# Kernel optimization log

Measured on AMD Instinct MI355X. Metric: run time of the kernel, lower is better.

The kernel has to match this reference:

```python
import jax, jax.numpy as jnp
import numpy as np

B, S, E = 4, 2048, 1024

def setup_inputs() -> dict:
    key = jax.random.key(0)
    ks = jax.random.split(key, 6)
    values = jax.random.normal(ks[0], (B, S, E), dtype=jnp.float32)
    keys_t = jax.random.normal(ks[1], (B, S, E), dtype=jnp.float32)
    query = jax.random.normal(ks[2], (B, S, E), dtype=jnp.float32)
    mask = jax.random.randint(ks[3], (B, 1, S), 0, 2, dtype=jnp.int32)
    W_out = jax.random.normal(ks[4], (E, E), dtype=jnp.float32) * (1.0 / np.sqrt(E))
    b_out = jax.random.normal(ks[5], (E,), dtype=jnp.float32) * 0.01
    return {"values": values, "keys": keys_t, "query": query, "mask": mask,
            "W_out": W_out, "b_out": b_out}

def reference(values, keys, query, mask, W_out, b_out):
    # scores: [B, S, S] = Q K^T / sqrt(embed_size)  (NOTE: module scales by
    # sqrt(embed_size), not sqrt(head_dim), and never applies q/k/v Linears)
    scale = 1.0 / jnp.sqrt(jnp.asarray(E, dtype=query.dtype))
    scores = jnp.einsum('bqe,bke->bqk', query, keys) * scale
    scores = jnp.where(mask == 0, -jnp.inf, scores)  # masked_fill(mask==0, -inf)
    attn = jax.nn.softmax(scores, axis=-1)
    out = jnp.einsum('bqk,bke->bqe', attn, values)
    # fc_out: torch Linear -> x @ W^T + b
    return out @ W_out.T + b_out
```

## Files before the change

### kernel.cpp

```cpp
#include <hip/hip_runtime.h>

#define BB 4
#define SS 2048
#define EE 1024

typedef _Float16 f16;
typedef _Float16 f16x4 __attribute__((ext_vector_type(4)));
typedef _Float16 f16x8 __attribute__((ext_vector_type(8)));
typedef float f32x4 __attribute__((ext_vector_type(4)));

typedef const __attribute__((address_space(1))) void* gas_ptr;
typedef __attribute__((address_space(3))) void* las_ptr;

__device__ __forceinline__ void gl_lds16(const void* g, void* l) {
  __builtin_amdgcn_global_load_lds((gas_ptr)g, (las_ptr)l, 16, 0, 0);
}

#define BAR() __builtin_amdgcn_s_barrier()
#define PRIO1() __builtin_amdgcn_s_setprio(1)
#define PRIO0() __builtin_amdgcn_s_setprio(0)
#define WAITV6() asm volatile("s_waitcnt vmcnt(6)" ::: "memory")
#define WAITV0() asm volatile("s_waitcnt vmcnt(0)" ::: "memory")

__global__ __launch_bounds__(256) void prep(const int* __restrict__ mask,
                                            int* __restrict__ pos,
                                            int2* __restrict__ cnt,
                                            f16* __restrict__ Kc,
                                            f16* __restrict__ Vc) {
  const int b = blockIdx.x, t = threadIdx.x;
  const int* mb = mask + b * SS;
  int4 a0 = ((const int4*)mb)[t * 2];
  int4 a1 = ((const int4*)mb)[t * 2 + 1];
  int m[8] = {a0.x, a0.y, a0.z, a0.w, a1.x, a1.y, a1.z, a1.w};
  int tot = 0;
#pragma unroll
  for (int j = 0; j < 8; ++j) tot += m[j];
  __shared__ int sc[256];
  sc[t] = tot;
  __syncthreads();
  for (int off = 1; off < 256; off <<= 1) {
    int v = (t >= off) ? sc[t - off] : 0;
    __syncthreads();
    sc[t] += v;
    __syncthreads();
  }
  const int count = sc[255];
  const int padded = (count + 127) & ~127;
  int run = sc[t] - tot;
#pragma unroll
  for (int j = 0; j < 8; ++j) {
    pos[b * SS + t * 8 + j] = run;
    run += m[j];
  }
  if (t == 0) cnt[b] = make_int2(count, padded);
  const int nz = (padded - count) * 128;
  f16x8 z = {};
  for (int i = t; i < nz; i += 256) {
    int r = count + (i >> 7), cc = i & 127;
    ((f16x8*)(Kc + ((long)b * SS + r) * EE))[cc] = z;
    ((f16x8*)(Vc + ((long)b * SS + r) * EE))[cc] = z;
  }
}

__global__ __launch_bounds__(256) void prep2(const float* __restrict__ Q,
                                             const float* __restrict__ W,
                                             const float* __restrict__ K,
                                             const float* __restrict__ V,
                                             const int* __restrict__ mask,
                                             const int* __restrict__ pos,
                                             const int2* __restrict__ cnt,
                                             f16* __restrict__ Qh,
                                             f16* __restrict__ Wh,
                                             f16* __restrict__ Kc,
                                             f16* __restrict__ Vc,
                                             float* __restrict__ rowsum,
                                             int* __restrict__ items,
                                             int* __restrict__ nit) {
  const int x = blockIdx.x, t = threadIdx.x;
  if (x < 4608) {
    const float* in = (x < 4096) ? Q : W;
    f16* out = (x < 4096) ? Qh : Wh;
    long i = (long)(x < 4096 ? x : x - 4096) * 256 + t;
    float4 v0 = ((const float4*)in)[i * 2];
    float4 v1 = ((const float4*)in)[i * 2 + 1];
    f16x8 o;
    o[0] = (f16)v0.x; o[1] = (f16)v0.y; o[2] = (f16)v0.z; o[3] = (f16)v0.w;
    o[4] = (f16)v1.x; o[5] = (f16)v1.y; o[6] = (f16)v1.z; o[7] = (f16)v1.w;
    ((f16x8*)out)[i] = o;
    return;
  }
  if (x == 4608) {
    float4 z = {0.f, 0.f, 0.f, 0.f};
#pragma unroll
    for (int r = 0; r < 8; ++r) ((float4*)rowsum)[t + r * 256] = z;
    return;
  }
  if (x == 4609) {
    if (t < 8) {
      int nbx[4];
#pragma unroll
      for (int zz = 0; zz < 4; ++zz) nbx[zz] = cnt[zz].y >> 7;
      int mxn = nbx[0];
#pragma unroll
      for (int zz = 1; zz < 4; ++zz) mxn = nbx[zz] > mxn ? nbx[zz] : mxn;
      const int mx = 6 * mxn;
      const int bz = t >> 1, half = t & 1;
      int g = 0;
      for (int q = 0; q < 4; ++q)
        for (int bx = 0; bx < nbx[bz]; ++bx)
          items[(g++ << 3) | t] = bx | ((half * 4 + q) << 8) | (bz << 16);
      for (int q = 0; q < 2; ++q)
        for (int bx = 0; bx < nbx[bz]; ++bx)
          items[(g++ << 3) | t] = bx | ((half * 2 + q) << 8) | (bz << 16) | (1 << 24);
      for (; g < mx; ++g) items[(g << 3) | t] = (3 << 24);
      if (t == 0) nit[0] = mx << 3;
    }
    return;
  }
  const int r = x - 4610, b = r >> 11, s = r & (SS - 1);
  if (!mask[b * SS + s]) return;
  const int p = pos[b * SS + s];
  float4 kv = ((const float4*)(K + ((long)b * SS + s) * EE))[t];
  float4 vv = ((const float4*)(V + ((long)b * SS + s) * EE))[t];
  f16x4 ko, vo;
  ko[0] = (f16)kv.x; ko[1] = (f16)kv.y; ko[2] = (f16)kv.z; ko[3] = (f16)kv.w;
  vo[0] = (f16)vv.x; vo[1] = (f16)vv.y; vo[2] = (f16)vv.z; vo[3] = (f16)vv.w;
  ((f16x4*)(Kc + ((long)b * SS + p) * EE))[t] = ko;
  ((f16x4*)(Vc + ((long)b * SS + p) * EE))[t] = vo;
}

__device__ __forceinline__ void stage64(const f16* g, long K, f16* l, int h, int t) {
  int rr = t >> 3, sp = t & 7;
  int row = h * 64 + rr;
  int sl = sp ^ (rr & 7);
  gl_lds16(g + (long)row * K + (sl << 3), (char*)l + ((row << 6) + (sp << 3)) * 2);
}

__device__ __forceinline__ void read_a(f16x8 (&d)[4][2], const f16* base, int q,
                                       int wm, int l15, int l4) {
#pragma unroll
  for (int mf = 0; mf < 4; ++mf)
#pragma unroll
    for (int kk = 0; kk < 2; ++kk) {
      int row = wm * 128 + (q * 4 + mf) * 16 + l15;
      int sl = kk * 4 + l4;
      d[mf][kk] = *(const f16x8*)(base + row * 64 + ((sl ^ (row & 7)) << 3));
    }
}

__device__ __forceinline__ void read_b1(f16x8 (&d)[2], const f16* base, int f,
                                        int wn, int l15, int l4) {
#pragma unroll
  for (int kk = 0; kk < 2; ++kk) {
    int row = wn * 32 + f * 16 + l15;
    int sl = kk * 4 + l4;
    d[kk] = *(const f16x8*)(base + row * 64 + ((sl ^ (row & 7)) << 3));
  }
}

__device__ __forceinline__ void mfma_n(f32x4 (&acc)[8][2], const f16x8 (&Af)[4][2],
                                       const f16x8 (&Bf)[2], int q, int f) {
#pragma unroll
  for (int mf = 0; mf < 4; ++mf)
#pragma unroll
    for (int kk = 0; kk < 2; ++kk)
      acc[q * 4 + mf][f] = __builtin_amdgcn_mfma_f32_16x16x32_f16(
          Af[mf][kk], Bf[kk], acc[q * 4 + mf][f], 0, 0, 0);
}

__device__ __forceinline__ void n128_core(f32x4 (&acc)[8][2], const f16* Ag,
                                          const f16* Bg, long L, int NT,
                                          f16* lds, int tid, int wm, int wn,
                                          int l15, int l4) {
  f16* As0 = lds;
  f16* As1 = lds + 16384;
  f16* Bs0 = lds + 32768;
  f16* Bs1 = lds + 40960;
  f16x8 a[4][2], b[2], b2[2];
  const int NIT = NT >> 1;

  stage64(Bg, L, Bs0, 0, tid); stage64(Bg, L, Bs0, 1, tid);
#pragma unroll
  for (int h = 0; h < 4; ++h) stage64(Ag, L, As0, h, tid);
  stage64(Bg + 64, L, Bs1, 0, tid); stage64(Bg + 64, L, Bs1, 1, tid);
#pragma unroll
  for (int h = 0; h < 4; ++h) stage64(Ag + 64, L, As1, h, tid);
  WAITV6();
  BAR();

  for (int i = 0; i < NIT; ++i) {
    int t2 = 2 * i + 2, t3 = 2 * i + 3;
    long k2 = (long)((t2 < NT) ? t2 : NT - 1) << 6;
    long k3 = (long)((t3 < NT) ? t3 : NT - 1) << 6;
    read_a(a, As0, 0, wm, l15, l4);
    read_b1(b, Bs0, 0, wn, l15, l4);
    BAR(); PRIO1(); mfma_n(acc, a, b, 0, 0); PRIO0(); BAR();
    read_b1(b2, Bs0, 1, wn, l15, l4);
    BAR(); PRIO1(); mfma_n(acc, a, b2, 0, 1); PRIO0(); BAR();
    read_a(a, As0, 1, wm, l15, l4);
    stage64(Bg + k2, L, Bs0, 0, tid); stage64(Bg + k2, L, Bs0, 1, tid);
    BAR(); PRIO1(); mfma_n(acc, a, b2, 1, 1); PRIO0(); BAR();
#pragma unroll
    for (int h = 0; h < 4; ++h) stage64(Ag + k2, L, As0, h, tid);
    BAR(); PRIO1(); mfma_n(acc, a, b, 1, 0); PRIO0();
    WAITV6();
    BAR();
    read_a(a, As1, 0, wm, l15, l4);
    read_b1(b, Bs1, 0, wn, l15, l4);
    BAR(); PRIO1(); mfma_n(acc, a, b, 0, 0); PRIO0(); BAR();
    read_b1(b2, Bs1, 1, wn, l15, l4);
    BAR(); PRIO1(); mfma_n(acc, a, b2, 0, 1); PRIO0(); BAR();
    read_a(a, As1, 1, wm, l15, l4);
    stage64(Bg + k3, L, Bs1, 0, tid); stage64(Bg + k3, L, Bs1, 1, tid);
    BAR(); PRIO1(); mfma_n(acc, a, b2, 1, 1); PRIO0(); BAR();
#pragma unroll
    for (int h = 0; h < 4; ++h) stage64(Ag + k3, L, As1, h, tid);
    BAR(); PRIO1(); mfma_n(acc, a, b, 1, 0); PRIO0();
    WAITV6();
    BAR();
  }
  WAITV0();
}

__global__ __launch_bounds__(512, 1) void uber(const f16* __restrict__ Qh,
                                               const f16* __restrict__ Kc,
                                               const f16* __restrict__ Vc,
                                               const f16* __restrict__ Wh,
                                               f16* __restrict__ P,
                                               f16* __restrict__ VWt,
                                               float* __restrict__ rowsum,
                                               const int2* __restrict__ cnt,
                                               const int* __restrict__ items,
                                               const int* __restrict__ nit) {
  extern __shared__ f16 lds[];
  const int tid = threadIdx.x;
  const int lane = tid & 63, wv = tid >> 6;
  const int wm = wv >> 2, wn = wv & 3;
  const int l15 = lane & 15, l4 = lane >> 4;
  const int n = nit[0];

  for (int idx = blockIdx.x; idx < n; idx += 256) {
    const int it = items[idx];
    const int kind = (it >> 24) & 3;
    if (kind == 3) continue;
    const int bx = it & 255, by = (it >> 8) & 255, bz = (it >> 16) & 255;
    const long m0 = (long)by * 256;
    const long n0 = (long)bx * 128;
    const f16* Ag = kind ? (Wh + m0 * EE) : (Qh + (long)bz * SS * EE + m0 * EE);
    const f16* Bg = (kind ? Vc : Kc) + (long)bz * SS * EE + n0 * EE;

    f32x4 acc[8][2] = {};
    n128_core(acc, Ag, Bg, EE, EE >> 6, lds, tid, wm, wn, l15, l4);

    const long crow = m0 + wm * 128 + l4 * 4;
    const long ccol = n0 + wn * 32 + l15;
    if (kind == 0) {
      const int count = cnt[bz].x;
      f16* Co = P + (long)bz * SS * SS;
      float* rs = rowsum + (bz << 11);
      const float scale = 1.0f / 32.0f;
      int mv[2];
#pragma unroll
      for (int nf = 0; nf < 2; ++nf) mv[nf] = (ccol + nf * 16) < count;
#pragma unroll
      for (int mf = 0; mf < 8; ++mf)
#pragma unroll
        for (int jj = 0; jj < 4; ++jj) {
          float rp = 0.f;
#pragma unroll
          for (int nf = 0; nf < 2; ++nf) {
            float p = mv[nf] ? __expf(acc[mf][nf][jj] * scale) : 0.f;
            Co[(crow + mf * 16 + jj) * SS + ccol + nf * 16] = (f16)p;
            rp += p;
          }
          rp += __shfl_xor(rp, 1); rp += __shfl_xor(rp, 2);
          rp += __shfl_xor(rp, 4); rp += __shfl_xor(rp, 8);
          if (l15 == 0) atomicAdd(&rs[crow + mf * 16 + jj], rp);
        }
    } else {
      f16* Co = VWt + (long)bz * EE * SS;
#pragma unroll
      for (int mf = 0; mf < 8; ++mf)
#pragma unroll
        for (int nf = 0; nf < 2; ++nf)
#pragma unroll
          for (int jj = 0; jj < 4; ++jj)
            Co[(crow + mf * 16 + jj) * SS + ccol + nf * 16] = (f16)acc[mf][nf][jj];
    }
  }
}

__global__ __launch_bounds__(512, 1) void pv128(const f16* __restrict__ P,
                                                const f16* __restrict__ VWt,
                                                float* __restrict__ out,
                                                const float* __restrict__ bias,
                                                const float* __restrict__ rowsum,
                                                const int2* __restrict__ cnt) {
  extern __shared__ f16 lds[];
  const int d = blockIdx.x;
  const int x = d & 7, r = d >> 3;
  const int bz = x >> 1;
  const int by = (x & 1) * 4 + (r & 3);
  const int bx = r >> 2;
  int2 cc = cnt[bz];
  const int padded = cc.y;
  if (padded <= 0) return;
  const long m0 = (long)by * 256;
  const long n0 = (long)bx * 128;
  const int tid = threadIdx.x;
  const int lane = tid & 63, wv = tid >> 6;
  const int wm = wv >> 2, wn = wv & 3;
  const int l15 = lane & 15, l4 = lane >> 4;
  const f16* Ag = P + (long)bz * SS * SS + m0 * SS;
  const f16* Bg = VWt + (long)bz * EE * SS + n0 * SS;

  f32x4 acc[8][2] = {};
  n128_core(acc, Ag, Bg, SS, padded >> 6, lds, tid, wm, wn, l15, l4);

  const long crow = m0 + wm * 128 + l4 * 4;
  const long ccol = n0 + wn * 32 + l15;
  float* Co = out + (long)bz * SS * EE;
  const float* rs = rowsum + (bz << 11);
  float bv[2];
#pragma unroll
  for (int nf = 0; nf < 2; ++nf) bv[nf] = bias[ccol + nf * 16];
#pragma unroll
  for (int mf = 0; mf < 8; ++mf)
#pragma unroll
    for (int jj = 0; jj < 4; ++jj) {
      float inv = 1.f / rs[crow + mf * 16 + jj];
#pragma unroll
      for (int nf = 0; nf < 2; ++nf)
        Co[(crow + mf * 16 + jj) * EE + ccol + nf * 16] =
            acc[mf][nf][jj] * inv + bv[nf];
    }
}

extern "C" void kernel_launch(void* const* d_in, const int* in_sizes, int n_in,
                              void* d_out, int out_size, void* d_ws, size_t ws_size,
                              hipStream_t stream) {
  const float* V = (const float*)d_in[0];
  const float* Kin = (const float*)d_in[1];
  const float* Q = (const float*)d_in[2];
  const int* mask = (const int*)d_in[3];
  const float* W = (const float*)d_in[4];
  const float* bias = (const float*)d_in[5];
  float* out = (float*)d_out;

  const long NE = (long)BB * SS * EE;
  f16* Qh = (f16*)d_ws;
  f16* Kc = Qh + NE;
  f16* Vc = Kc + NE;
  f16* Wh = Vc + NE;
  f16* VWt = Wh + (long)EE * EE;
  f16* P = VWt + NE;
  float* rowsum = (float*)(P + (long)BB * SS * SS);
  int* pos = (int*)(rowsum + (long)BB * SS);
  int2* cnt = (int2*)(pos + (long)BB * SS);
  int* items = (int*)(cnt + BB);
  int* nit = items + 1024;

  const size_t LDS_N = 98304;
  hipFuncSetAttribute((const void*)uber, hipFuncAttributeMaxDynamicSharedMemorySize, LDS_N);
  hipFuncSetAttribute((const void*)pv128, hipFuncAttributeMaxDynamicSharedMemorySize, LDS_N);

  prep<<<BB, 256, 0, stream>>>(mask, pos, cnt, Kc, Vc);
  prep2<<<4610 + BB * SS, 256, 0, stream>>>(Q, W, Kin, V, mask, pos, cnt,
                                            Qh, Wh, Kc, Vc, rowsum, items, nit);
  uber<<<256, 512, LDS_N, stream>>>(Qh, Kc, Vc, Wh, P, VWt, rowsum, cnt, items, nit);
  pv128<<<256, 512, LDS_N, stream>>>(P, VWt, out, bias, rowsum, cnt);
}
```

Measured before the change: 102.6 us.

## Widen uber GEMM tiles to 256x256 with new pipelined core

Replaces the 256x128 GEMM core in the persistent uber kernel with a 256x256 core (g256_core). Each wave now computes a 128x64 sub-tile, and A and B are double-buffered in 128KB of LDS. Key/value padding and work-item counts move to 256-column granularity. The aim is to raise arithmetic intensity and cut redundant A-tile loads. In exchange it uses more accumulator registers and more LDS, adds padding work when the mask count is not a multiple of 256, and leaves fewer items to balance across the 256 blocks.

```diff
diff --git a/kernel.cpp b/kernel.cpp
--- a/kernel.cpp
+++ b/kernel.cpp
@@ -19,7 +19,9 @@
 #define BAR() __builtin_amdgcn_s_barrier()
 #define PRIO1() __builtin_amdgcn_s_setprio(1)
 #define PRIO0() __builtin_amdgcn_s_setprio(0)
+#define WAITV8() asm volatile("s_waitcnt vmcnt(8)" ::: "memory")
 #define WAITV6() asm volatile("s_waitcnt vmcnt(6)" ::: "memory")
+#define WAITV4() asm volatile("s_waitcnt vmcnt(4)" ::: "memory")
 #define WAITV0() asm volatile("s_waitcnt vmcnt(0)" ::: "memory")
 
 __global__ __launch_bounds__(256) void prep(const int* __restrict__ mask,
@@ -45,7 +47,7 @@
     __syncthreads();
   }
   const int count = sc[255];
-  const int padded = (count + 127) & ~127;
+  const int padded = (count + 255) & ~255;
   int run = sc[t] - tot;
 #pragma unroll
   for (int j = 0; j < 8; ++j) {
@@ -99,7 +101,7 @@
     if (t < 8) {
       int nbx[4];
 #pragma unroll
-      for (int zz = 0; zz < 4; ++zz) nbx[zz] = cnt[zz].y >> 7;
+      for (int zz = 0; zz < 4; ++zz) nbx[zz] = cnt[zz].y >> 8;
       int mxn = nbx[0];
 #pragma unroll
       for (int zz = 1; zz < 4; ++zz) mxn = nbx[zz] > mxn ? nbx[zz] : mxn;
@@ -148,6 +150,18 @@
     }
 }
 
+__device__ __forceinline__ void read_b2(f16x8 (&d)[2][2], const f16* base, int nh,
+                                        int wn, int l15, int l4) {
+#pragma unroll
+  for (int nf = 0; nf < 2; ++nf)
+#pragma unroll
+    for (int kk = 0; kk < 2; ++kk) {
+      int row = wn * 64 + (nh * 2 + nf) * 16 + l15;
+      int sl = kk * 4 + l4;
+      d[nf][kk] = *(const f16x8*)(base + row * 64 + ((sl ^ (row & 7)) << 3));
+    }
+}
+
 __device__ __forceinline__ void read_b1(f16x8 (&d)[2], const f16* base, int f,
                                         int wn, int l15, int l4) {
 #pragma unroll
@@ -158,6 +172,18 @@
   }
 }
 
+__device__ __forceinline__ void mfma_q(f32x4 (&acc)[8][4], const f16x8 (&Af)[4][2],
+                                       const f16x8 (&Bf)[2][2], int q, int nh) {
+#pragma unroll
+  for (int mf = 0; mf < 4; ++mf)
+#pragma unroll
+    for (int nf = 0; nf < 2; ++nf)
+#pragma unroll
+      for (int kk = 0; kk < 2; ++kk)
+        acc[q * 4 + mf][nh * 2 + nf] = __builtin_amdgcn_mfma_f32_16x16x32_f16(
+            Af[mf][kk], Bf[nf][kk], acc[q * 4 + mf][nh * 2 + nf], 0, 0, 0);
+}
+
 __device__ __forceinline__ void mfma_n(f32x4 (&acc)[8][2], const f16x8 (&Af)[4][2],
                                        const f16x8 (&Bf)[2], int q, int f) {
 #pragma unroll
@@ -166,6 +192,64 @@
     for (int kk = 0; kk < 2; ++kk)
       acc[q * 4 + mf][f] = __builtin_amdgcn_mfma_f32_16x16x32_f16(
           Af[mf][kk], Bf[kk], acc[q * 4 + mf][f], 0, 0, 0);
+}
+
+__device__ __forceinline__ void g256_core(f32x4 (&acc)[8][4], const f16* Ag,
+                                          const f16* Bg, long L, int NT,
+                                          f16* lds, int tid, int wm, int wn,
+                                          int l15, int l4) {
+  f16* As0 = lds;
+  f16* As1 = lds + 16384;
+  f16* Bs0 = lds + 32768;
+  f16* Bs1 = lds + 49152;
+  f16x8 a[4][2], b[2][2], b2[2][2];
+  const int NIT = NT >> 1;
+
+#pragma unroll
+  for (int h = 0; h < 4; ++h) stage64(Bg, L, Bs0, h, tid);
+#pragma unroll
+  for (int h = 0; h < 4; ++h) stage64(Ag, L, As0, h, tid);
+#pragma unroll
+  for (int h = 0; h < 4; ++h) stage64(Bg + 64, L, Bs1, h, tid);
+#pragma unroll
+  for (int h = 0; h < 4; ++h) stage64(Ag + 64, L, As1, h, tid);
+  WAITV8();
+  BAR();
+
+  for (int i = 0; i < NIT; ++i) {
+    int t2 = 2 * i + 2, t3 = 2 * i + 3;
+    long k2 = (long)((t2 < NT) ? t2 : NT - 1) << 6;
+    long k3 = (long)((t3 < NT) ? t3 : NT - 1) << 6;
+    read_a(a, As0, 0, wm, l15, l4);
+    read_b2(b, Bs0, 0, wn, l15, l4);
+    BAR(); PRIO1(); mfma_q(acc, a, b, 0, 0); PRIO0(); BAR();
+    read_b2(b2, Bs0, 1, wn, l15, l4);
+    BAR(); PRIO1(); mfma_q(acc, a, b2, 0, 1); PRIO0(); BAR();
+    read_a(a, As0, 1, wm, l15, l4);
+    stage64(Bg + k2, L, Bs0, 0, tid); stage64(Bg + k2, L, Bs0, 1, tid);
+    BAR(); PRIO1(); mfma_q(acc, a, b2, 1, 1); PRIO0(); BAR();
+    stage64(Bg + k2, L, Bs0, 2, tid); stage64(Bg + k2, L, Bs0, 3, tid);
+    BAR(); PRIO1(); mfma_q(acc, a, b, 1, 0); PRIO0();
+    WAITV4();
+    BAR();
+    read_a(a, As1, 0, wm, l15, l4);
+    read_b2(b, Bs1, 0, wn, l15, l4);
+    stage64(Ag + k2, L, As0, 0, tid); stage64(Ag + k2, L, As0, 1, tid);
+    BAR(); PRIO1(); mfma_q(acc, a, b, 0, 0); PRIO0(); BAR();
+    read_b2(b2, Bs1, 1, wn, l15, l4);
+    stage64(Ag + k2, L, As0, 2, tid); stage64(Ag + k2, L, As0, 3, tid);
+    BAR(); PRIO1(); mfma_q(acc, a, b2, 0, 1); PRIO0(); BAR();
+    read_a(a, As1, 1, wm, l15, l4);
+    stage64(Bg + k3, L, Bs1, 0, tid); stage64(Bg + k3, L, Bs1, 1, tid);
+    BAR(); PRIO1(); mfma_q(acc, a, b2, 1, 1); PRIO0(); BAR();
+    stage64(Bg + k3, L, Bs1, 2, tid); stage64(Bg + k3, L, Bs1, 3, tid);
+    stage64(Ag + k3, L, As1, 0, tid); stage64(Ag + k3, L, As1, 1, tid);
+    stage64(Ag + k3, L, As1, 2, tid); stage64(Ag + k3, L, As1, 3, tid);
+    BAR(); PRIO1(); mfma_q(acc, a, b, 1, 0); PRIO0();
+    WAITV8();
+    BAR();
+  }
+  WAITV0();
 }
 
 __device__ __forceinline__ void n128_core(f32x4 (&acc)[8][2], const f16* Ag,
@@ -245,30 +329,30 @@
     if (kind == 3) continue;
     const int bx = it & 255, by = (it >> 8) & 255, bz = (it >> 16) & 255;
     const long m0 = (long)by * 256;
-    const long n0 = (long)bx * 128;
+    const long n0 = (long)bx * 256;
     const f16* Ag = kind ? (Wh + m0 * EE) : (Qh + (long)bz * SS * EE + m0 * EE);
     const f16* Bg = (kind ? Vc : Kc) + (long)bz * SS * EE + n0 * EE;
 
-    f32x4 acc[8][2] = {};
-    n128_core(acc, Ag, Bg, EE, EE >> 6, lds, tid, wm, wn, l15, l4);
+    f32x4 acc[8][4] = {};
+    g256_core(acc, Ag, Bg, EE, EE >> 6, lds, tid, wm, wn, l15, l4);
 
     const long crow = m0 + wm * 128 + l4 * 4;
-    const long ccol = n0 + wn * 32 + l15;
+    const long ccol = n0 + wn * 64 + l15;
     if (kind == 0) {
       const int count = cnt[bz].x;
       f16* Co = P + (long)bz * SS * SS;
       float* rs = rowsum + (bz << 11);
       const float scale = 1.0f / 32.0f;
-      int mv[2];
-#pragma unroll
-      for (int nf = 0; nf < 2; ++nf) mv[nf] = (ccol + nf * 16) < count;
+      int mv[4];
+#pragma unroll
+      for (int nf = 0; nf < 4; ++nf) mv[nf] = (ccol + nf * 16) < count;
 #pragma unroll
       for (int mf = 0; mf < 8; ++mf)
 #pragma unroll
         for (int jj = 0; jj < 4; ++jj) {
           float rp = 0.f;
 #pragma unroll
-          for (int nf = 0; nf < 2; ++nf) {
+          for (int nf = 0; nf < 4; ++nf) {
             float p = mv[nf] ? __expf(acc[mf][nf][jj] * scale) : 0.f;
             Co[(crow + mf * 16 + jj) * SS + ccol + nf * 16] = (f16)p;
             rp += p;
@@ -282,7 +366,7 @@
 #pragma unroll
       for (int mf = 0; mf < 8; ++mf)
 #pragma unroll
-        for (int nf = 0; nf < 2; ++nf)
+        for (int nf = 0; nf < 4; ++nf)
 #pragma unroll
           for (int jj = 0; jj < 4; ++jj)
             Co[(crow + mf * 16 + jj) * SS + ccol + nf * 16] = (f16)acc[mf][nf][jj];
@@ -360,13 +444,13 @@
   int* items = (int*)(cnt + BB);
   int* nit = items + 1024;
 
-  const size_t LDS_N = 98304;
-  hipFuncSetAttribute((const void*)uber, hipFuncAttributeMaxDynamicSharedMemorySize, LDS_N);
+  const size_t LDS_Q = 131072, LDS_N = 98304;
+  hipFuncSetAttribute((const void*)uber, hipFuncAttributeMaxDynamicSharedMemorySize, LDS_Q);
   hipFuncSetAttribute((const void*)pv128, hipFuncAttributeMaxDynamicSharedMemorySize, LDS_N);
 
   prep<<<BB, 256, 0, stream>>>(mask, pos, cnt, Kc, Vc);
   prep2<<<4610 + BB * SS, 256, 0, stream>>>(Q, W, Kin, V, mask, pos, cnt,
                                             Qh, Wh, Kc, Vc, rowsum, items, nit);
-  uber<<<256, 512, LDS_N, stream>>>(Qh, Kc, Vc, Wh, P, VWt, rowsum, cnt, items, nit);
+  uber<<<256, 512, LDS_Q, stream>>>(Qh, Kc, Vc, Wh, P, VWt, rowsum, cnt, items, nit);
   pv128<<<256, 512, LDS_N, stream>>>(P, VWt, out, bias, rowsum, cnt);
 }
```

After: 97.59 us. 4.9% less time.
